# Kernel tuning notes

Hardware: AMD Instinct MI355X
Metric: run time of the kernel (lower is better)

## Reference

```python
import jax, jax.numpy as jnp
import numpy as np

# DeepSeek-V2-Lite MoE dims
E = 64      # n_routed_experts
H = 2048    # hidden_size
I = 1408    # moe_intermediate_size
K = 6       # num_experts_per_tok (top-k)
T = 1024    # tokens
C = 256     # per-expert capacity (expected load T*K/E = 96; 256 is ample, no drops with seed 0)


def setup_inputs() -> dict:
    key = jax.random.key(0)
    k1, k2, k3, k4 = jax.random.split(key, 4)
    return {
        "hidden_states": jax.random.normal(k1, (T, H), jnp.float32),
        "gate_w": jax.random.normal(k2, (H, E), jnp.float32) * 0.02,   # LiteLinear(H->E), no bias
        "w1": jax.random.normal(k3, (E, H, I), jnp.float32) * 0.02,    # experts_w1
        "w2": jax.random.normal(k4, (E, I, H), jnp.float32) * 0.02,    # experts_w2
    }


def _moe(x, gate_w, w1, w2):
    # Router: softmax gate + top-k + renormalize (vLLM fused_moe renormalize=True)
    logits = x @ gate_w                                    # [T, E]
    probs = jax.nn.softmax(logits, axis=-1)
    topk_w, topk_idx = jax.lax.top_k(probs, K)             # [T, K]
    topk_w = topk_w / jnp.sum(topk_w, axis=-1, keepdims=True)

    # Dispatch: flatten (token, k) pairs, compute slot position within each expert
    P = T * K
    e_p = topk_idx.reshape(P)                              # expert id per pair
    onehot = (e_p[:, None] == jnp.arange(E)[None, :]).astype(jnp.int32)  # [P, E]
    pos = jnp.cumsum(onehot, axis=0) - 1                   # running count per expert
    pos = jnp.take_along_axis(pos, e_p[:, None], axis=1)[:, 0]           # [P]
    valid = pos < C
    pos_c = jnp.where(valid, pos, 0)
    fvalid = valid[:, None].astype(x.dtype)

    x_pair = jnp.repeat(x, K, axis=0)                      # [P, H]
    xe = jnp.zeros((E, C, H), x.dtype).at[e_p, pos_c].add(x_pair * fvalid)  # [E, C, H]

    # Grouped expert GEMMs: silu(x @ w1) @ w2
    h = jax.nn.silu(jnp.einsum('ech,ehi->eci', xe, w1))    # [E, C, I]
    ye = jnp.einsum('eci,eih->ech', h, w2)                 # [E, C, H]

    # Combine: gather back per pair, weight by routing prob, sum over k
    y_pair = ye[e_p, pos_c] * fvalid                       # [P, H]
    out = (y_pair.reshape(T, K, H) * topk_w[..., None]).sum(axis=1)
    return out


def reference(hidden_states, gate_w, w1, w2):
    return _moe(hidden_states, gate_w, w1, w2)
```

## Files before the change

### kernel.cpp

```cpp
#include <hip/hip_runtime.h>

#define T_TOK 1024
#define H_DIM 2048
#define I_DIM 1408
#define E_NUM 64
#define K_TOP 6
#define CAP   256
#define P_NUM (T_TOK * K_TOP)
#define ROWS_MAX 7168

typedef __bf16 bf16x8 __attribute__((ext_vector_type(8)));
typedef float  f32x4  __attribute__((ext_vector_type(4)));

__global__ void zero_out_kernel(float* __restrict__ out) {
    int i = blockIdx.x * 256 + threadIdx.x;
    ((f32x4*)out)[i] = (f32x4){0.f, 0.f, 0.f, 0.f};
}

__global__ void zerocnt_kernel(int* __restrict__ cnt) {
    if (threadIdx.x < E_NUM) cnt[threadIdx.x] = 0;
}

__global__ __launch_bounds__(256) void router_kernel(
        const float* __restrict__ x, const float* __restrict__ gw,
        float* __restrict__ tw, int* __restrict__ ti, __bf16* __restrict__ xb)
{
    const int t0  = blockIdx.x * 4;
    const int tid = threadIdx.x;
    __shared__ float xs[4][H_DIM];
    __shared__ float part[4][4][E_NUM];

    #pragma unroll
    for (int tt = 0; tt < 4; ++tt) {
        #pragma unroll
        for (int i = 0; i < 8; ++i) {
            float v = x[(size_t)(t0 + tt) * H_DIM + i * 256 + tid];
            xs[tt][i * 256 + tid] = v;
            xb[(size_t)(t0 + tt) * H_DIM + i * 256 + tid] = (__bf16)v;
        }
    }
    __syncthreads();

    const int e = tid & 63, q = tid >> 6;
    float a0 = 0.f, a1 = 0.f, a2 = 0.f, a3 = 0.f;
    for (int hh = q * 512; hh < q * 512 + 512; ++hh) {
        float g = gw[hh * E_NUM + e];
        a0 += xs[0][hh] * g; a1 += xs[1][hh] * g;
        a2 += xs[2][hh] * g; a3 += xs[3][hh] * g;
    }
    part[q][0][e] = a0; part[q][1][e] = a1; part[q][2][e] = a2; part[q][3][e] = a3;
    __syncthreads();

    const int tt = q;
    float l = part[0][tt][e] + part[1][tt][e] + part[2][tt][e] + part[3][tt][e];
    float m = l;
    #pragma unroll
    for (int s = 32; s; s >>= 1) m = fmaxf(m, __shfl_xor(m, s));
    float p = __expf(l - m);
    float sum = p;
    #pragma unroll
    for (int s = 32; s; s >>= 1) sum += __shfl_xor(sum, s);
    float prob = p / sum;

    float v = prob, wsum = 0.f;
    float tv[K_TOP]; int tix[K_TOP];
    #pragma unroll
    for (int k = 0; k < K_TOP; ++k) {
        float bv = v; int bi = e;
        #pragma unroll
        for (int s = 32; s; s >>= 1) {
            float ov = __shfl_xor(bv, s); int oi = __shfl_xor(bi, s);
            if (ov > bv || (ov == bv && oi < bi)) { bv = ov; bi = oi; }
        }
        tv[k] = bv; tix[k] = bi; wsum += bv;
        if (e == bi) v = -1.0f;
    }
    if (e == 0) {
        #pragma unroll
        for (int k = 0; k < K_TOP; ++k) {
            tw[(t0 + tt) * K_TOP + k] = tv[k] / wsum;
            ti[(t0 + tt) * K_TOP + k] = tix[k];
        }
    }
}

__global__ void dispatch_kernel(const int* __restrict__ ti, int* __restrict__ cnt,
                                int* __restrict__ list) {
    int p = blockIdx.x * 256 + threadIdx.x;
    if (p < P_NUM) {
        int e = ti[p];
        int slot = atomicAdd(&cnt[e], 1);
        if (slot < CAP) list[e * CAP + slot] = p;
    }
}

__global__ void scan_kernel(const int* __restrict__ cnt, int* __restrict__ base) {
    if (threadIdx.x == 0) {
        int acc = 0;
        for (int e = 0; e < E_NUM; ++e) {
            base[e] = acc;
            int c = cnt[e]; if (c > CAP) c = CAP;
            acc += (c + 15) & ~15;
        }
    }
}

__global__ __launch_bounds__(256, 2) void gemm1_kernel(
        const float* __restrict__ w1, const __bf16* __restrict__ xb,
        const int* __restrict__ cnt, const int* __restrict__ base,
        const int* __restrict__ list, __bf16* __restrict__ hbuf)
{
    const int e  = blockIdx.z;
    const int m0 = blockIdx.y * 128;
    const int nb = blockIdx.x * 128;

    int rows = cnt[e]; if (rows > CAP) rows = CAP;
    const int rows_pad = (rows + 15) & ~15;
    if (m0 >= rows_pad) return;
    int mcount = rows_pad - m0; if (mcount > 128) mcount = 128;
    const int nmf = mcount >> 4;
    const int hb = base[e];

    __shared__ __attribute__((aligned(16))) __bf16 As[128][72];
    __shared__ int ts[128];

    const int tid = threadIdx.x;
    if (tid < 128) {
        int slot = m0 + tid;
        ts[tid] = (slot < rows) ? (list[e * CAP + slot] / K_TOP) : 0;
    }
    __syncthreads();

    const int lane = tid & 63;
    const int wv   = tid >> 6;
    const int l15  = lane & 15;
    const int lg   = lane >> 4;
    const int nw   = nb + wv * 32;

    const int sm = tid >> 3;
    const int sk = (tid & 7) << 3;

    const __bf16* ap[4];
    #pragma unroll
    for (int it = 0; it < 4; ++it)
        ap[it] = xb + (size_t)ts[it * 32 + sm] * H_DIM + sk;

    const float* wbase = w1 + (size_t)e * H_DIM * I_DIM
                            + (size_t)(lg * 8) * I_DIM + (nw + l15);

    f32x4 acc[8][2];
    #pragma unroll
    for (int m = 0; m < 8; ++m) {
        acc[m][0] = (f32x4){0.f, 0.f, 0.f, 0.f};
        acc[m][1] = (f32x4){0.f, 0.f, 0.f, 0.f};
    }

    for (int k0 = 0; k0 < H_DIM; k0 += 64) {
        bf16x8 bfr[2][2];
        #pragma unroll
        for (int ks = 0; ks < 2; ++ks) {
            const float* bp = wbase + (size_t)(k0 + ks * 32) * I_DIM;
            #pragma unroll
            for (int nf = 0; nf < 2; ++nf) {
                #pragma unroll
                for (int j = 0; j < 8; ++j)
                    bfr[ks][nf][j] = (__bf16)bp[(size_t)j * I_DIM + nf * 16];
            }
        }
        __syncthreads();
        #pragma unroll
        for (int it = 0; it < 4; ++it) {
            bf16x8 v = *(const bf16x8*)(ap[it] + k0);
            *(bf16x8*)(&As[it * 32 + sm][sk]) = v;
        }
        __syncthreads();
        #pragma unroll
        for (int ks = 0; ks < 2; ++ks) {
            #pragma unroll
            for (int m = 0; m < 8; ++m) {
                if (m < nmf) {
                    bf16x8 a = *(const bf16x8*)(&As[m * 16 + l15][ks * 32 + lg * 8]);
                    acc[m][0] = __builtin_amdgcn_mfma_f32_16x16x32_bf16(a, bfr[ks][0], acc[m][0], 0, 0, 0);
                    acc[m][1] = __builtin_amdgcn_mfma_f32_16x16x32_bf16(a, bfr[ks][1], acc[m][1], 0, 0, 0);
                }
            }
        }
    }

    #pragma unroll
    for (int m = 0; m < 8; ++m) {
        if (m < nmf) {
            #pragma unroll
            for (int nf = 0; nf < 2; ++nf) {
                #pragma unroll
                for (int j = 0; j < 4; ++j) {
                    int row = m * 16 + lg * 4 + j;
                    int col = nw + nf * 16 + l15;
                    float v = acc[m][nf][j];
                    float s = v / (1.0f + __expf(-v));
                    hbuf[(size_t)(hb + m0 + row) * I_DIM + col] = (__bf16)s;
                }
            }
        }
    }
}

__global__ __launch_bounds__(256, 2) void gemm2_kernel(
        const float* __restrict__ w2, const __bf16* __restrict__ hbuf,
        const int* __restrict__ cnt, const int* __restrict__ base,
        const int* __restrict__ list, const float* __restrict__ tw,
        float* __restrict__ out)
{
    const int e  = blockIdx.z;
    const int m0 = blockIdx.y * 128;
    const int nb = blockIdx.x * 128;

    int rows = cnt[e]; if (rows > CAP) rows = CAP;
    const int rows_pad = (rows + 15) & ~15;
    if (m0 >= rows_pad) return;
    int mcount = rows_pad - m0; if (mcount > 128) mcount = 128;
    const int nmf = mcount >> 4;
    const int hb = base[e];

    __shared__ __attribute__((aligned(16))) __bf16 As[128][72];
    __shared__ int ps[128];
    __shared__ float tws[128];

    const int tid = threadIdx.x;
    if (tid < 128) {
        int slot = m0 + tid;
        int p = (slot < rows) ? list[e * CAP + slot] : -1;
        ps[tid] = p;
        tws[tid] = (p >= 0) ? tw[p] : 0.f;
    }

    const int lane = tid & 63;
    const int wv   = tid >> 6;
    const int l15  = lane & 15;
    const int lg   = lane >> 4;
    const int nw   = nb + wv * 32;

    const int sm = tid >> 3;
    const int sk = (tid & 7) << 3;

    const __bf16* abase = hbuf + (size_t)(hb + m0 + sm) * I_DIM + sk;
    const float*  wbase = w2 + (size_t)e * I_DIM * H_DIM
                             + (size_t)(lg * 8) * H_DIM + (nw + l15);

    f32x4 acc[8][2];
    #pragma unroll
    for (int m = 0; m < 8; ++m) {
        acc[m][0] = (f32x4){0.f, 0.f, 0.f, 0.f};
        acc[m][1] = (f32x4){0.f, 0.f, 0.f, 0.f};
    }

    for (int k0 = 0; k0 < I_DIM; k0 += 64) {
        bf16x8 bfr[2][2];
        #pragma unroll
        for (int ks = 0; ks < 2; ++ks) {
            const float* bp = wbase + (size_t)(k0 + ks * 32) * H_DIM;
            #pragma unroll
            for (int nf = 0; nf < 2; ++nf) {
                #pragma unroll
                for (int j = 0; j < 8; ++j)
                    bfr[ks][nf][j] = (__bf16)bp[(size_t)j * H_DIM + nf * 16];
            }
        }
        __syncthreads();
        #pragma unroll
        for (int it = 0; it < 4; ++it) {
            bf16x8 v = *(const bf16x8*)(abase + (size_t)(it * 32) * I_DIM + k0);
            *(bf16x8*)(&As[it * 32 + sm][sk]) = v;
        }
        __syncthreads();
        #pragma unroll
        for (int ks = 0; ks < 2; ++ks) {
            #pragma unroll
            for (int m = 0; m < 8; ++m) {
                if (m < nmf) {
                    bf16x8 a = *(const bf16x8*)(&As[m * 16 + l15][ks * 32 + lg * 8]);
                    acc[m][0] = __builtin_amdgcn_mfma_f32_16x16x32_bf16(a, bfr[ks][0], acc[m][0], 0, 0, 0);
                    acc[m][1] = __builtin_amdgcn_mfma_f32_16x16x32_bf16(a, bfr[ks][1], acc[m][1], 0, 0, 0);
                }
            }
        }
    }

    #pragma unroll
    for (int m = 0; m < 8; ++m) {
        if (m < nmf) {
            #pragma unroll
            for (int nf = 0; nf < 2; ++nf) {
                #pragma unroll
                for (int j = 0; j < 4; ++j) {
                    int row = m * 16 + lg * 4 + j;
                    int p = ps[row];
                    if (p >= 0) {
                        int t = p / K_TOP;
                        float v = acc[m][nf][j] * tws[row];
                        atomicAdd(&out[(size_t)t * H_DIM + (nw + nf * 16 + l15)], v);
                    }
                }
            }
        }
    }
}

extern "C" void kernel_launch(void* const* d_in, const int* in_sizes, int n_in,
                              void* d_out, int out_size, void* d_ws, size_t ws_size,
                              hipStream_t stream) {
    const float* x  = (const float*)d_in[0];
    const float* gw = (const float*)d_in[1];
    const float* w1 = (const float*)d_in[2];
    const float* w2 = (const float*)d_in[3];
    float* out = (float*)d_out;

    char* ws = (char*)d_ws;
    int*    cnt  = (int*)ws;
    int*    base = (int*)(ws + 256);
    int*    list = (int*)(ws + 512);
    float*  tw   = (float*)(ws + 66048);
    int*    ti   = (int*)(ws + 90624);
    __bf16* xb   = (__bf16*)(ws + 131072);
    __bf16* hbuf = (__bf16*)(ws + 4325376);

    hipLaunchKernelGGL(zero_out_kernel, dim3(T_TOK * H_DIM / 4 / 256), dim3(256), 0, stream, out);
    hipLaunchKernelGGL(zerocnt_kernel, dim3(1), dim3(64), 0, stream, cnt);
    hipLaunchKernelGGL(router_kernel, dim3(T_TOK / 4), dim3(256), 0, stream,
                       x, gw, tw, ti, xb);
    hipLaunchKernelGGL(dispatch_kernel, dim3((P_NUM + 255) / 256), dim3(256), 0, stream,
                       ti, cnt, list);
    hipLaunchKernelGGL(scan_kernel, dim3(1), dim3(64), 0, stream, cnt, base);
    hipLaunchKernelGGL(gemm1_kernel, dim3(I_DIM / 128, 2, E_NUM), dim3(256), 0, stream,
                       w1, xb, cnt, base, list, hbuf);
    hipLaunchKernelGGL(gemm2_kernel, dim3(H_DIM / 128, 2, E_NUM), dim3(256), 0, stream,
                       w2, hbuf, cnt, base, list, tw, out);
}
```

Baseline: 509.4 us.

## Stage fp32 expert weights through swizzled LDS with vectorized loads

Both expert GEMMs used to read fp32 weights with scalar, strided per-lane loads, one element per row per lane. They now issue coalesced 16-byte row loads, pack pairs to bf16, and write them into an XOR-swizzled shared-memory B tile that the MFMA fragments read back. The A and B global loads are also issued before the first barrier so their latency overlaps. The aim is to cut memory transactions on the weight stream, which dominates traffic. This adds LDS usage and an extra LDS round trip, and occupancy hints are raised to 3 blocks per SM.

After: 464.9 us. -8.7%, faster.

```diff
diff --git a/kernel.cpp b/kernel.cpp
--- a/kernel.cpp
+++ b/kernel.cpp
@@ -11,6 +11,13 @@
 
 typedef __bf16 bf16x8 __attribute__((ext_vector_type(8)));
 typedef float  f32x4  __attribute__((ext_vector_type(4)));
+typedef unsigned int uint32x2 __attribute__((ext_vector_type(2)));
+
+__device__ inline unsigned pack2bf16(float a, float b) {
+    unsigned short au = __builtin_bit_cast(unsigned short, (__bf16)a);
+    unsigned short bu = __builtin_bit_cast(unsigned short, (__bf16)b);
+    return (unsigned)au | ((unsigned)bu << 16);
+}
 
 __global__ void zero_out_kernel(float* __restrict__ out) {
     int i = blockIdx.x * 256 + threadIdx.x;
@@ -105,7 +112,9 @@
     }
 }
 
-__global__ __launch_bounds__(256, 2) void gemm1_kernel(
+#define B_LDB 36
+
+__global__ __launch_bounds__(256, 3) void gemm1_kernel(
         const float* __restrict__ w1, const __bf16* __restrict__ xb,
         const int* __restrict__ cnt, const int* __restrict__ base,
         const int* __restrict__ list, __bf16* __restrict__ hbuf)
@@ -122,6 +131,7 @@
     const int hb = base[e];
 
     __shared__ __attribute__((aligned(16))) __bf16 As[128][72];
+    __shared__ __attribute__((aligned(16))) unsigned Bs[128 * B_LDB];
     __shared__ int ts[128];
 
     const int tid = threadIdx.x;
@@ -135,18 +145,26 @@
     const int wv   = tid >> 6;
     const int l15  = lane & 15;
     const int lg   = lane >> 4;
-    const int nw   = nb + wv * 32;
 
     const int sm = tid >> 3;
     const int sk = (tid & 7) << 3;
-
     const __bf16* ap[4];
     #pragma unroll
     for (int it = 0; it < 4; ++it)
         ap[it] = xb + (size_t)ts[it * 32 + sm] * H_DIM + sk;
 
-    const float* wbase = w1 + (size_t)e * H_DIM * I_DIM
-                            + (size_t)(lg * 8) * I_DIM + (nw + l15);
+    const int c4 = tid & 31;
+    const int kb = tid >> 5;
+    const int Xw = 4 * ((c4 ^ (c4 >> 3)) & 7);
+    const float* bload = w1 + (size_t)e * H_DIM * I_DIM + (nb + 4 * c4);
+
+    int cB0 = wv * 32 + l15;
+    int cB1 = cB0 + 16;
+    int c4r0 = cB0 >> 2, c4r1 = cB1 >> 2;
+    const int Xr0 = 4 * ((c4r0 ^ (c4r0 >> 3)) & 7);
+    const int Xr1 = 4 * ((c4r1 ^ (c4r1 >> 3)) & 7);
+    const unsigned* bfp0 = Bs + cB0 * B_LDB;
+    const unsigned* bfp1 = Bs + cB1 * B_LDB;
 
     f32x4 acc[8][2];
     #pragma unroll
@@ -156,37 +174,51 @@
     }
 
     for (int k0 = 0; k0 < H_DIM; k0 += 64) {
-        bf16x8 bfr[2][2];
+        f32x4 f[8];
+        const float* bp = bload + (size_t)(k0 + 4 * kb) * I_DIM;
+        #pragma unroll
+        for (int r = 0; r < 4; ++r) f[r] = *(const f32x4*)(bp + (size_t)r * I_DIM);
+        const float* bp2 = bp + (size_t)32 * I_DIM;
+        #pragma unroll
+        for (int r = 0; r < 4; ++r) f[4 + r] = *(const f32x4*)(bp2 + (size_t)r * I_DIM);
+        bf16x8 av[4];
+        #pragma unroll
+        for (int it = 0; it < 4; ++it) av[it] = *(const bf16x8*)(ap[it] + k0);
+
+        __syncthreads();
+        #pragma unroll
+        for (int it = 0; it < 4; ++it)
+            *(bf16x8*)(&As[it * 32 + sm][sk]) = av[it];
+        #pragma unroll
+        for (int b = 0; b < 2; ++b) {
+            #pragma unroll
+            for (int i = 0; i < 4; ++i) {
+                unsigned lo = pack2bf16(f[4 * b + 0][i], f[4 * b + 1][i]);
+                unsigned hi = pack2bf16(f[4 * b + 2][i], f[4 * b + 3][i]);
+                int c = 4 * c4 + i;
+                int p = 2 * kb + 16 * b;
+                *(uint32x2*)(&Bs[c * B_LDB + (p ^ Xw)]) = (uint32x2){lo, hi};
+            }
+        }
+        __syncthreads();
+
         #pragma unroll
         for (int ks = 0; ks < 2; ++ks) {
-            const float* bp = wbase + (size_t)(k0 + ks * 32) * I_DIM;
-            #pragma unroll
-            for (int nf = 0; nf < 2; ++nf) {
-                #pragma unroll
-                for (int j = 0; j < 8; ++j)
-                    bfr[ks][nf][j] = (__bf16)bp[(size_t)j * I_DIM + nf * 16];
-            }
-        }
-        __syncthreads();
-        #pragma unroll
-        for (int it = 0; it < 4; ++it) {
-            bf16x8 v = *(const bf16x8*)(ap[it] + k0);
-            *(bf16x8*)(&As[it * 32 + sm][sk]) = v;
-        }
-        __syncthreads();
-        #pragma unroll
-        for (int ks = 0; ks < 2; ++ks) {
+            int pbase = ks * 16 + lg * 4;
+            bf16x8 b0 = *(const bf16x8*)(bfp0 + (pbase ^ Xr0));
+            bf16x8 b1 = *(const bf16x8*)(bfp1 + (pbase ^ Xr1));
             #pragma unroll
             for (int m = 0; m < 8; ++m) {
                 if (m < nmf) {
                     bf16x8 a = *(const bf16x8*)(&As[m * 16 + l15][ks * 32 + lg * 8]);
-                    acc[m][0] = __builtin_amdgcn_mfma_f32_16x16x32_bf16(a, bfr[ks][0], acc[m][0], 0, 0, 0);
-                    acc[m][1] = __builtin_amdgcn_mfma_f32_16x16x32_bf16(a, bfr[ks][1], acc[m][1], 0, 0, 0);
+                    acc[m][0] = __builtin_amdgcn_mfma_f32_16x16x32_bf16(a, b0, acc[m][0], 0, 0, 0);
+                    acc[m][1] = __builtin_amdgcn_mfma_f32_16x16x32_bf16(a, b1, acc[m][1], 0, 0, 0);
                 }
             }
         }
     }
 
+    const int nw = nb + wv * 32;
     #pragma unroll
     for (int m = 0; m < 8; ++m) {
         if (m < nmf) {
@@ -205,7 +237,7 @@
     }
 }
 
-__global__ __launch_bounds__(256, 2) void gemm2_kernel(
+__global__ __launch_bounds__(256, 3) void gemm2_kernel(
         const float* __restrict__ w2, const __bf16* __restrict__ hbuf,
         const int* __restrict__ cnt, const int* __restrict__ base,
         const int* __restrict__ list, const float* __restrict__ tw,
@@ -223,6 +255,7 @@
     const int hb = base[e];
 
     __shared__ __attribute__((aligned(16))) __bf16 As[128][72];
+    __shared__ __attribute__((aligned(16))) unsigned Bs[128 * B_LDB];
     __shared__ int ps[128];
     __shared__ float tws[128];
 
@@ -238,14 +271,23 @@
     const int wv   = tid >> 6;
     const int l15  = lane & 15;
     const int lg   = lane >> 4;
-    const int nw   = nb + wv * 32;
 
     const int sm = tid >> 3;
     const int sk = (tid & 7) << 3;
-
     const __bf16* abase = hbuf + (size_t)(hb + m0 + sm) * I_DIM + sk;
-    const float*  wbase = w2 + (size_t)e * I_DIM * H_DIM
-                             + (size_t)(lg * 8) * H_DIM + (nw + l15);
+
+    const int c4 = tid & 31;
+    const int kb = tid >> 5;
+    const int Xw = 4 * ((c4 ^ (c4 >> 3)) & 7);
+    const float* bload = w2 + (size_t)e * I_DIM * H_DIM + (nb + 4 * c4);
+
+    int cB0 = wv * 32 + l15;
+    int cB1 = cB0 + 16;
+    int c4r0 = cB0 >> 2, c4r1 = cB1 >> 2;
+    const int Xr0 = 4 * ((c4r0 ^ (c4r0 >> 3)) & 7);
+    const int Xr1 = 4 * ((c4r1 ^ (c4r1 >> 3)) & 7);
+    const unsigned* bfp0 = Bs + cB0 * B_LDB;
+    const unsigned* bfp1 = Bs + cB1 * B_LDB;
 
     f32x4 acc[8][2];
     #pragma unroll
@@ -255,37 +297,52 @@
     }
 
     for (int k0 = 0; k0 < I_DIM; k0 += 64) {
-        bf16x8 bfr[2][2];
+        f32x4 f[8];
+        const float* bp = bload + (size_t)(k0 + 4 * kb) * H_DIM;
+        #pragma unroll
+        for (int r = 0; r < 4; ++r) f[r] = *(const f32x4*)(bp + (size_t)r * H_DIM);
+        const float* bp2 = bp + (size_t)32 * H_DIM;
+        #pragma unroll
+        for (int r = 0; r < 4; ++r) f[4 + r] = *(const f32x4*)(bp2 + (size_t)r * H_DIM);
+        bf16x8 av[4];
+        #pragma unroll
+        for (int it = 0; it < 4; ++it)
+            av[it] = *(const bf16x8*)(abase + (size_t)(it * 32) * I_DIM + k0);
+
+        __syncthreads();
+        #pragma unroll
+        for (int it = 0; it < 4; ++it)
+            *(bf16x8*)(&As[it * 32 + sm][sk]) = av[it];
+        #pragma unroll
+        for (int b = 0; b < 2; ++b) {
+            #pragma unroll
+            for (int i = 0; i < 4; ++i) {
+                unsigned lo = pack2bf16(f[4 * b + 0][i], f[4 * b + 1][i]);
+                unsigned hi = pack2bf16(f[4 * b + 2][i], f[4 * b + 3][i]);
+                int c = 4 * c4 + i;
+                int p = 2 * kb + 16 * b;
+                *(uint32x2*)(&Bs[c * B_LDB + (p ^ Xw)]) = (uint32x2){lo, hi};
+            }
+        }
+        __syncthreads();
+
         #pragma unroll
         for (int ks = 0; ks < 2; ++ks) {
-            const float* bp = wbase + (size_t)(k0 + ks * 32) * H_DIM;
-            #pragma unroll
-            for (int nf = 0; nf < 2; ++nf) {
-                #pragma unroll
-                for (int j = 0; j < 8; ++j)
-                    bfr[ks][nf][j] = (__bf16)bp[(size_t)j * H_DIM + nf * 16];
-            }
-        }
-        __syncthreads();
-        #pragma unroll
-        for (int it = 0; it < 4; ++it) {
-            bf16x8 v = *(const bf16x8*)(abase + (size_t)(it * 32) * I_DIM + k0);
-            *(bf16x8*)(&As[it * 32 + sm][sk]) = v;
-        }
-        __syncthreads();
-        #pragma unroll
-        for (int ks = 0; ks < 2; ++ks) {
+            int pbase = ks * 16 + lg * 4;
+            bf16x8 b0 = *(const bf16x8*)(bfp0 + (pbase ^ Xr0));
+            bf16x8 b1 = *(const bf16x8*)(bfp1 + (pbase ^ Xr1));
             #pragma unroll
             for (int m = 0; m < 8; ++m) {
                 if (m < nmf) {
                     bf16x8 a = *(const bf16x8*)(&As[m * 16 + l15][ks * 32 + lg * 8]);
-                    acc[m][0] = __builtin_amdgcn_mfma_f32_16x16x32_bf16(a, bfr[ks][0], acc[m][0], 0, 0, 0);
-                    acc[m][1] = __builtin_amdgcn_mfma_f32_16x16x32_bf16(a, bfr[ks][1], acc[m][1], 0, 0, 0);
+                    acc[m][0] = __builtin_amdgcn_mfma_f32_16x16x32_bf16(a, b0, acc[m][0], 0, 0, 0);
+                    acc[m][1] = __builtin_amdgcn_mfma_f32_16x16x32_bf16(a, b1, acc[m][1], 0, 0, 0);
                 }
             }
         }
     }
 
+    const int nw = nb + wv * 32;
     #pragma unroll
     for (int m = 0; m < 8; ++m) {
         if (m < nmf) {
```
